# Optimization experiments

Hardware: AMD Instinct MI355X
Metric: run time of the kernel (lower is better)

Reference implementation:

```python
import jax, jax.numpy as jnp
import numpy as np

N_NODES = 50000
N_EDGES = 800000
IN_CH = 128
HID = 16
HEADS = 8
OUT_CH = 40
NEG_SLOPE = 0.2  # PyG GATConv default leaky_relu slope


def segment_softmax(logits, seg, num_segments):
    # logits: [E, H], softmax over edges sharing the same destination node
    m = jax.ops.segment_max(logits, seg, num_segments=num_segments)  # [N, H]
    e = jnp.exp(logits - m[seg])
    s = jax.ops.segment_sum(e, seg, num_segments=num_segments)  # [N, H]
    return e / s[seg]


def gat_conv(x, edge_index, W, att_src, att_dst, bias, heads, ch, concat):
    N = x.shape[0]
    h = (x @ W).reshape(N, heads, ch)                     # [N, H, C]
    a_src = jnp.sum(h * att_src, axis=-1)                 # [N, H]
    a_dst = jnp.sum(h * att_dst, axis=-1)                 # [N, H]
    src, dst = edge_index[0], edge_index[1]
    alpha = jax.nn.leaky_relu(a_src[src] + a_dst[dst], NEG_SLOPE)  # [E, H]
    alpha = segment_softmax(alpha, dst, N)                # [E, H]
    msg = h[src] * alpha[:, :, None]                      # [E, H, C]
    out = jax.ops.segment_sum(msg, dst, num_segments=N)   # [N, H, C]
    out = out.reshape(N, heads * ch) if concat else out.mean(axis=1)
    return out + bias


def setup_inputs() -> dict:
    key = jax.random.key(0)
    ks = jax.random.split(key, 10)
    g = 0.1
    return {
        "x": jax.random.normal(ks[0], (N_NODES, IN_CH), jnp.float32),
        "edge_index": jax.random.randint(ks[1], (2, N_EDGES), 0, N_NODES, jnp.int32),
        "W1": jax.random.normal(ks[2], (IN_CH, HEADS * HID), jnp.float32) * g,
        "att_src1": jax.random.normal(ks[3], (HEADS, HID), jnp.float32) * g,
        "att_dst1": jax.random.normal(ks[4], (HEADS, HID), jnp.float32) * g,
        "b1": jnp.zeros((HEADS * HID,), jnp.float32),
        "W2": jax.random.normal(ks[5], (HEADS * HID, OUT_CH), jnp.float32) * g,
        "att_src2": jax.random.normal(ks[6], (1, OUT_CH), jnp.float32) * g,
        "att_dst2": jax.random.normal(ks[7], (1, OUT_CH), jnp.float32) * g,
        "b2": jnp.zeros((OUT_CH,), jnp.float32),
    }


def reference(x, edge_index, W1, att_src1, att_dst1, b1, W2, att_src2, att_dst2, b2):
    # layer 1: GATConv(in->hid, heads=8, concat) + ELU (dropout is identity in eval)
    h = gat_conv(x, edge_index, W1, att_src1, att_dst1, b1, HEADS, HID, concat=True)
    h = jax.nn.elu(h)
    # layer 2: GATConv(hid*heads->out, heads=1, concat=False)
    out = gat_conv(h, edge_index, W2, att_src2, att_dst2, b2, 1, OUT_CH, concat=False)
    return out
```

## Files before the change

### kernel.cpp

```cpp
#include <hip/hip_runtime.h>
#include <hip/hip_bf16.h>
#include <math.h>

#define N_NODES 50000
#define E_EDGES 800000
#define IN_CH 128
#define HIDX 128
#define OUT_CH 40
#define NEG_SLOPE 0.2f
#define RANK_BLKS 160
#define EDGES_PER_RANK_BLK 5000
#define GEMM_BLKS_X 782
#define PAD_SHIFT 6
#define POISON_I ((int)0xAAAAAAAA)

static __device__ __forceinline__ unsigned int f2bf_pk(float lo, float hi) {
    unsigned int ul = __float_as_uint(lo);
    unsigned int uh = __float_as_uint(hi);
    ul = (ul + 0x7fffu + ((ul >> 16) & 1u)) >> 16;
    uh = (uh + 0x7fffu + ((uh >> 16) & 1u)) >> 16;
    return ul | (uh << 16);
}
static __device__ __forceinline__ float bf2f(unsigned short u) {
    return __uint_as_float(((unsigned int)u) << 16);
}


__global__ __launch_bounds__(256) void gemm1_kernel(
    const float* __restrict__ x, const float* __restrict__ W1,
    const float* __restrict__ as1, const float* __restrict__ ad1,
    unsigned short* __restrict__ H1, float* __restrict__ A1s, float* __restrict__ A1d,
    const int* __restrict__ ei, int* __restrict__ deg, unsigned short* __restrict__ csr_pad)
{
    int tid = threadIdx.x;
    int bid = blockIdx.x;

    if (bid < RANK_BLKS) {
        int start = bid * EDGES_PER_RANK_BLK;
        int endv  = start + EDGES_PER_RANK_BLK;
        if (endv > E_EDGES) endv = E_EDGES;
        for (int base = start; base < endv; base += 1024) {
            int e0 = base + tid;
            int e1 = e0 + 256, e2 = e0 + 512, e3 = e0 + 768;
            bool v0 = e0 < endv, v1 = e1 < endv, v2 = e2 < endv, v3 = e3 < endv;
            int d0 = 0, d1 = 0, d2 = 0, d3 = 0;
            int s0 = 0, s1 = 0, s2 = 0, s3 = 0;
            if (v0) { d0 = ei[E_EDGES + e0]; s0 = ei[e0]; }
            if (v1) { d1 = ei[E_EDGES + e1]; s1 = ei[e1]; }
            if (v2) { d2 = ei[E_EDGES + e2]; s2 = ei[e2]; }
            if (v3) { d3 = ei[E_EDGES + e3]; s3 = ei[e3]; }
            int r0, r1, r2, r3;
            if (v0) r0 = atomicAdd(&deg[d0], 1) - POISON_I;
            if (v1) r1 = atomicAdd(&deg[d1], 1) - POISON_I;
            if (v2) r2 = atomicAdd(&deg[d2], 1) - POISON_I;
            if (v3) r3 = atomicAdd(&deg[d3], 1) - POISON_I;
            if (v0) csr_pad[(d0 << PAD_SHIFT) + r0] = (unsigned short)s0;
            if (v1) csr_pad[(d1 << PAD_SHIFT) + r1] = (unsigned short)s1;
            if (v2) csr_pad[(d2 << PAD_SHIFT) + r2] = (unsigned short)s2;
            if (v3) csr_pad[(d3 << PAD_SHIFT) + r3] = (unsigned short)s3;
        }
        return;
    }

    __shared__ float Ws[32 * 68];
    __shared__ float XT[64 * 40];
    int g = bid - RANK_BLKS;
    int rowbase = (g >> 1) * 64;
    int cb = g & 1;

    const float4* W4 = (const float4*)W1;
    const float4* x4 = (const float4*)x;

    int cg = tid & 15;
    int rg = tid >> 4;
    int c0 = cg * 4;
    int r0 = rg * 4;
    float acc[4][4];
#pragma unroll
    for (int i = 0; i < 4; i++)
#pragma unroll
        for (int j = 0; j < 4; j++) acc[i][j] = 0.f;

#pragma unroll
    for (int kh = 0; kh < 4; kh++) {
        if (kh) __syncthreads();
#pragma unroll
        for (int i = 0; i < 2; i++) {
            int f = i * 256 + tid;
            int k = f >> 4, c4 = f & 15;
            *(float4*)(Ws + k * 68 + c4 * 4) = W4[(kh * 32 + k) * 32 + cb * 16 + c4];
        }
#pragma unroll
        for (int i = 0; i < 2; i++) {
            int f = i * 256 + tid;
            int r = f >> 3, c4 = f & 7;
            int gr = rowbase + r; if (gr >= N_NODES) gr = N_NODES - 1;
            *(float4*)(XT + r * 40 + c4 * 4) = x4[gr * 32 + kh * 8 + c4];
        }
        __syncthreads();

        for (int k = 0; k < 32; k += 4) {
            float4 xv[4];
#pragma unroll
            for (int i = 0; i < 4; i++) xv[i] = *(const float4*)(XT + (r0 + i) * 40 + k);
#pragma unroll
            for (int kk = 0; kk < 4; kk++) {
                float4 wv = *(const float4*)(Ws + (k + kk) * 68 + c0);
#pragma unroll
                for (int i = 0; i < 4; i++) {
                    float xs = (kk == 0) ? xv[i].x : (kk == 1) ? xv[i].y : (kk == 2) ? xv[i].z : xv[i].w;
                    acc[i][0] += xs * wv.x; acc[i][1] += xs * wv.y;
                    acc[i][2] += xs * wv.z; acc[i][3] += xs * wv.w;
                }
            }
        }
    }

    int gc0 = cb * 64 + c0;
    int hh = gc0 >> 4;
    float asp[4] = {0, 0, 0, 0}, adp[4] = {0, 0, 0, 0};
#pragma unroll
    for (int j = 0; j < 4; j++) {
        float va = as1[gc0 + j];
        float vd = ad1[gc0 + j];
#pragma unroll
        for (int i = 0; i < 4; i++) { asp[i] += acc[i][j] * va; adp[i] += acc[i][j] * vd; }
    }
#pragma unroll
    for (int i = 0; i < 4; i++) {
        asp[i] += __shfl_xor(asp[i], 1); asp[i] += __shfl_xor(asp[i], 2);
        adp[i] += __shfl_xor(adp[i], 1); adp[i] += __shfl_xor(adp[i], 2);
    }
#pragma unroll
    for (int i = 0; i < 4; i++) {
        int gr = rowbase + r0 + i;
        if (gr < N_NODES) {
            uint2 v;
            v.x = f2bf_pk(acc[i][0], acc[i][1]);
            v.y = f2bf_pk(acc[i][2], acc[i][3]);
            *(uint2*)(H1 + gr * 128 + gc0) = v;
            if ((cg & 3) == 0) {
                A1s[gr * 8 + hh] = asp[i];
                A1d[gr * 8 + hh] = adp[i];
            }
        }
    }
}


__global__ __launch_bounds__(256) void agg1_kernel(
    const int* __restrict__ deg, const unsigned short* __restrict__ csr_pad,
    const float* __restrict__ A1s, const float* __restrict__ A1d,
    const unsigned short* __restrict__ H1, const float* __restrict__ b1,
    unsigned short* __restrict__ X2)
{
    int gwave = (blockIdx.x * blockDim.x + threadIdx.x) >> 6;
    int lane = threadIdx.x & 63;
    if (gwave >= N_NODES) return;
    int node = gwave;
    int beg = node << PAD_SHIFT;
    int end = beg + (deg[node] - POISON_I);
    int half = lane >> 5;
    int li = lane & 31;
    int head = li >> 2;
    int c0 = li * 4;
    float ad = A1d[node * 8 + head];
    float acc0 = 0.f, acc1 = 0.f, acc2 = 0.f, acc3 = 0.f, sumw = 0.f;
    for (int p = beg; p < end; p += 16) {
        int s[8]; float a[8]; ushort4 u[8]; bool v[8];
#pragma unroll
        for (int t = 0; t < 8; t++) {
            int e = p + 2 * t + half;
            v[t] = e < end;
            s[t] = csr_pad[v[t] ? e : beg];
        }
#pragma unroll
        for (int t = 0; t < 8; t++) a[t] = A1s[s[t] * 8 + head];
#pragma unroll
        for (int t = 0; t < 8; t++) u[t] = *(const ushort4*)(H1 + s[t] * 128 + c0);
#pragma unroll
        for (int t = 0; t < 8; t++) {
            float z = a[t] + ad; z = z >= 0.f ? z : NEG_SLOPE * z;
            float w = v[t] ? __expf(z) : 0.f;
            acc0 += w * bf2f(u[t].x);
            acc1 += w * bf2f(u[t].y);
            acc2 += w * bf2f(u[t].z);
            acc3 += w * bf2f(u[t].w);
            sumw += w;
        }
    }
    acc0 += __shfl_xor(acc0, 32);
    acc1 += __shfl_xor(acc1, 32);
    acc2 += __shfl_xor(acc2, 32);
    acc3 += __shfl_xor(acc3, 32);
    sumw += __shfl_xor(sumw, 32);
    if (half == 0) {
        float inv = (end > beg) ? 1.0f / sumw : 0.0f;
        float4 bv = *(const float4*)(b1 + c0);
        float o0 = acc0 * inv + bv.x;
        float o1 = acc1 * inv + bv.y;
        float o2 = acc2 * inv + bv.z;
        float o3 = acc3 * inv + bv.w;
        o0 = o0 > 0.f ? o0 : expm1f(o0);
        o1 = o1 > 0.f ? o1 : expm1f(o1);
        o2 = o2 > 0.f ? o2 : expm1f(o2);
        o3 = o3 > 0.f ? o3 : expm1f(o3);
        uint2 ov;
        ov.x = f2bf_pk(o0, o1);
        ov.y = f2bf_pk(o2, o3);
        *(uint2*)(X2 + node * 128 + c0) = ov;
    }
}


__global__ __launch_bounds__(256) void gemm2_kernel(
    const unsigned short* __restrict__ X2, const float* __restrict__ W2,
    const float* __restrict__ as2, const float* __restrict__ ad2,
    unsigned short* __restrict__ H2, float* __restrict__ A2s, float* __restrict__ A2d)
{
    __shared__ float Ws[128 * 40];
    __shared__ float XS[64 * 132];
    int tid = threadIdx.x;
    int rowbase = blockIdx.x * 64;

#pragma unroll
    for (int i = 0; i < 20; i++) Ws[i * 256 + tid] = W2[i * 256 + tid];

    const uint2* x2v = (const uint2*)X2;
#pragma unroll
    for (int i = 0; i < 8; i++) {
        int f = i * 256 + tid;
        int r = f >> 5, c4 = f & 31;
        int gr = rowbase + r; if (gr >= N_NODES) gr = N_NODES - 1;
        uint2 pk = x2v[gr * 32 + c4];
        float* dst = XS + r * 132 + c4 * 4;
        dst[0] = bf2f((unsigned short)(pk.x & 0xffff));
        dst[1] = bf2f((unsigned short)(pk.x >> 16));
        dst[2] = bf2f((unsigned short)(pk.y & 0xffff));
        dst[3] = bf2f((unsigned short)(pk.y >> 16));
    }
    __syncthreads();

    int q = tid & 3, r = tid >> 2;
    float acc[10];
#pragma unroll
    for (int j = 0; j < 10; j++) acc[j] = 0.f;
    for (int k = 0; k < 128; k += 4) {
        float4 xv = *(const float4*)(XS + r * 132 + k);
#pragma unroll
        for (int kk = 0; kk < 4; kk++) {
            float xs = (kk == 0) ? xv.x : (kk == 1) ? xv.y : (kk == 2) ? xv.z : xv.w;
#pragma unroll
            for (int j = 0; j < 10; j++) acc[j] += xs * Ws[(k + kk) * 40 + q * 10 + j];
        }
    }
    float asum = 0.f, dsum = 0.f;
#pragma unroll
    for (int j = 0; j < 10; j++) {
        asum += acc[j] * as2[q * 10 + j];
        dsum += acc[j] * ad2[q * 10 + j];
    }
    asum += __shfl_xor(asum, 1); asum += __shfl_xor(asum, 2);
    dsum += __shfl_xor(dsum, 1); dsum += __shfl_xor(dsum, 2);
    int gr = rowbase + r;
    if (gr < N_NODES) {
#pragma unroll
        for (int t = 0; t < 5; t++)
            *(unsigned int*)(H2 + gr * 40 + q * 10 + t * 2) = f2bf_pk(acc[t * 2], acc[t * 2 + 1]);
        if (q == 0) { A2s[gr] = asum; A2d[gr] = dsum; }
    }
}


__global__ __launch_bounds__(256) void agg2_kernel(
    const int* __restrict__ deg, const unsigned short* __restrict__ csr_pad,
    const float* __restrict__ A2s, const float* __restrict__ A2d,
    const unsigned short* __restrict__ H2, const float* __restrict__ b2,
    float* __restrict__ out)
{
    int gwave = (blockIdx.x * blockDim.x + threadIdx.x) >> 6;
    int lane = threadIdx.x & 63;
    if (gwave >= N_NODES) return;
    int node = gwave;
    int beg = node << PAD_SHIFT;
    int end = beg + (deg[node] - POISON_I);
    int half = lane >> 5;
    int li = lane & 31;
    bool act = li < 20;
    int c0 = li * 2;
    int cc = act ? c0 : 0;
    float ad = A2d[node];
    float acc0 = 0.f, acc1 = 0.f, sumw = 0.f;
    for (int p = beg; p < end; p += 16) {
        int s[8]; float a[8]; ushort2 u[8]; bool v[8];
#pragma unroll
        for (int t = 0; t < 8; t++) {
            int e = p + 2 * t + half;
            v[t] = e < end;
            s[t] = csr_pad[v[t] ? e : beg];
        }
#pragma unroll
        for (int t = 0; t < 8; t++) a[t] = A2s[s[t]];
#pragma unroll
        for (int t = 0; t < 8; t++) u[t] = *(const ushort2*)(H2 + s[t] * OUT_CH + cc);
#pragma unroll
        for (int t = 0; t < 8; t++) {
            float z = a[t] + ad; z = z >= 0.f ? z : NEG_SLOPE * z;
            float w = v[t] ? __expf(z) : 0.f;
            acc0 += w * bf2f(u[t].x);
            acc1 += w * bf2f(u[t].y);
            sumw += w;
        }
    }
    acc0 += __shfl_xor(acc0, 32);
    acc1 += __shfl_xor(acc1, 32);
    sumw += __shfl_xor(sumw, 32);
    if (half == 0 && act) {
        float inv = (end > beg) ? 1.0f / sumw : 0.0f;
        float o0 = acc0 * inv + b2[c0];
        float o1 = acc1 * inv + b2[c0 + 1];
        float2 ov = {o0, o1};
        *(float2*)(out + node * OUT_CH + c0) = ov;
    }
}


extern "C" void kernel_launch(void* const* d_in, const int* in_sizes, int n_in,
                              void* d_out, int out_size, void* d_ws, size_t ws_size,
                              hipStream_t stream) {
    const float* x   = (const float*)d_in[0];
    const int*   ei  = (const int*)d_in[1];
    const float* W1  = (const float*)d_in[2];
    const float* as1 = (const float*)d_in[3];
    const float* ad1 = (const float*)d_in[4];
    const float* b1  = (const float*)d_in[5];
    const float* W2  = (const float*)d_in[6];
    const float* as2 = (const float*)d_in[7];
    const float* ad2 = (const float*)d_in[8];
    const float* b2  = (const float*)d_in[9];
    float* out = (float*)d_out;

    char* ws = (char*)d_ws;
    size_t off = 0;
    auto alloc = [&](size_t bytes) {
        void* p = ws + off;
        off += (bytes + 255) & ~size_t(255);
        return p;
    };
    unsigned short* H1 = (unsigned short*)alloc((size_t)N_NODES * 128 * 2);
    unsigned short* X2 = (unsigned short*)alloc((size_t)N_NODES * 128 * 2);
    unsigned short* H2 = (unsigned short*)alloc((size_t)N_NODES * OUT_CH * 2);
    float* A1s    = (float*)alloc((size_t)N_NODES * 8 * 4);
    float* A1d    = (float*)alloc((size_t)N_NODES * 8 * 4);
    float* A2s    = (float*)alloc((size_t)N_NODES * 4);
    float* A2d    = (float*)alloc((size_t)N_NODES * 4);
    int* deg      = (int*)alloc((size_t)N_NODES * 4);
    unsigned short* csr_pad = (unsigned short*)alloc((size_t)N_NODES * 64 * 2);


    gemm1_kernel<<<RANK_BLKS + GEMM_BLKS_X * 2, 256, 0, stream>>>(
        x, W1, as1, ad1, H1, A1s, A1d, ei, deg, csr_pad);

    agg1_kernel<<<(N_NODES + 3) / 4, 256, 0, stream>>>(deg, csr_pad, A1s, A1d, H1, b1, X2);

    gemm2_kernel<<<(N_NODES + 63) / 64, 256, 0, stream>>>(X2, W2, as2, ad2, H2, A2s, A2d);
    agg2_kernel<<<(N_NODES + 3) / 4, 256, 0, stream>>>(deg, csr_pad, A2s, A2d, H2, b2, out);
}
```

Measured before the change: 217.5 us.

## Fuse layer-1 aggregation with layer-2 GEMM through shared memory

Merges the layer-1 attention aggregation and the layer-2 projection into one kernel: each block aggregates 32 nodes (8 per wave) into bf16 rows in LDS, then multiplies them by a transposed W2 tile held in LDS. This removes the X2 global round trip and one kernel launch. In exchange each block does more serial work per wave, reloads and transposes W2 in every block, and uses more shared memory, which may lower occupancy for the latency-bound gather phase.

```diff
diff --git a/kernel.cpp b/kernel.cpp
--- a/kernel.cpp
+++ b/kernel.cpp
@@ -11,6 +11,7 @@
 #define RANK_BLKS 160
 #define EDGES_PER_RANK_BLK 5000
 #define GEMM_BLKS_X 782
+#define FUSE_BLKS 1563
 #define PAD_SHIFT 6
 #define POISON_I ((int)0xAAAAAAAA)
 
@@ -20,6 +21,10 @@
     ul = (ul + 0x7fffu + ((ul >> 16) & 1u)) >> 16;
     uh = (uh + 0x7fffu + ((uh >> 16) & 1u)) >> 16;
     return ul | (uh << 16);
+}
+static __device__ __forceinline__ unsigned short f2bf1(float v) {
+    unsigned int u = __float_as_uint(v);
+    return (unsigned short)((u + 0x7fffu + ((u >> 16) & 1u)) >> 16);
 }
 static __device__ __forceinline__ float bf2f(unsigned short u) {
     return __uint_as_float(((unsigned int)u) << 16);
@@ -71,9 +76,9 @@
     const float4* W4 = (const float4*)W1;
     const float4* x4 = (const float4*)x;
 
-    int cg = tid & 15;
+    int cg_ = tid & 15;
     int rg = tid >> 4;
-    int c0 = cg * 4;
+    int c0 = cg_ * 4;
     int r0 = rg * 4;
     float acc[4][4];
 #pragma unroll
@@ -139,7 +144,7 @@
             v.x = f2bf_pk(acc[i][0], acc[i][1]);
             v.y = f2bf_pk(acc[i][2], acc[i][3]);
             *(uint2*)(H1 + gr * 128 + gc0) = v;
-            if ((cg & 3) == 0) {
+            if ((cg_ & 3) == 0) {
                 A1s[gr * 8 + hh] = asp[i];
                 A1d[gr * 8 + hh] = adp[i];
             }
@@ -148,126 +153,132 @@
 }
 
 
-__global__ __launch_bounds__(256) void agg1_kernel(
+__global__ __launch_bounds__(256) void fused_ag_kernel(
     const int* __restrict__ deg, const unsigned short* __restrict__ csr_pad,
     const float* __restrict__ A1s, const float* __restrict__ A1d,
     const unsigned short* __restrict__ H1, const float* __restrict__ b1,
-    unsigned short* __restrict__ X2)
+    const float* __restrict__ W2, const float* __restrict__ as2,
+    const float* __restrict__ ad2,
+    unsigned short* __restrict__ H2, float* __restrict__ A2s, float* __restrict__ A2d)
 {
-    int gwave = (blockIdx.x * blockDim.x + threadIdx.x) >> 6;
-    int lane = threadIdx.x & 63;
-    if (gwave >= N_NODES) return;
-    int node = gwave;
-    int beg = node << PAD_SHIFT;
-    int end = beg + (deg[node] - POISON_I);
+    __shared__ float WsT[40 * 132];
+    __shared__ unsigned int x2s[32 * 68];
+    int tid = threadIdx.x;
+    int bid = blockIdx.x;
+    int wid = tid >> 6;
+    int lane = tid & 63;
     int half = lane >> 5;
     int li = lane & 31;
-    int head = li >> 2;
-    int c0 = li * 4;
-    float ad = A1d[node * 8 + head];
-    float acc0 = 0.f, acc1 = 0.f, acc2 = 0.f, acc3 = 0.f, sumw = 0.f;
-    for (int p = beg; p < end; p += 16) {
-        int s[8]; float a[8]; ushort4 u[8]; bool v[8];
-#pragma unroll
-        for (int t = 0; t < 8; t++) {
-            int e = p + 2 * t + half;
-            v[t] = e < end;
-            s[t] = csr_pad[v[t] ? e : beg];
-        }
-#pragma unroll
-        for (int t = 0; t < 8; t++) a[t] = A1s[s[t] * 8 + head];
-#pragma unroll
-        for (int t = 0; t < 8; t++) u[t] = *(const ushort4*)(H1 + s[t] * 128 + c0);
-#pragma unroll
-        for (int t = 0; t < 8; t++) {
-            float z = a[t] + ad; z = z >= 0.f ? z : NEG_SLOPE * z;
-            float w = v[t] ? __expf(z) : 0.f;
-            acc0 += w * bf2f(u[t].x);
-            acc1 += w * bf2f(u[t].y);
-            acc2 += w * bf2f(u[t].z);
-            acc3 += w * bf2f(u[t].w);
-            sumw += w;
-        }
-    }
-    acc0 += __shfl_xor(acc0, 32);
-    acc1 += __shfl_xor(acc1, 32);
-    acc2 += __shfl_xor(acc2, 32);
-    acc3 += __shfl_xor(acc3, 32);
-    sumw += __shfl_xor(sumw, 32);
-    if (half == 0) {
-        float inv = (end > beg) ? 1.0f / sumw : 0.0f;
-        float4 bv = *(const float4*)(b1 + c0);
-        float o0 = acc0 * inv + bv.x;
-        float o1 = acc1 * inv + bv.y;
-        float o2 = acc2 * inv + bv.z;
-        float o3 = acc3 * inv + bv.w;
-        o0 = o0 > 0.f ? o0 : expm1f(o0);
-        o1 = o1 > 0.f ? o1 : expm1f(o1);
-        o2 = o2 > 0.f ? o2 : expm1f(o2);
-        o3 = o3 > 0.f ? o3 : expm1f(o3);
-        uint2 ov;
-        ov.x = f2bf_pk(o0, o1);
-        ov.y = f2bf_pk(o2, o3);
-        *(uint2*)(X2 + node * 128 + c0) = ov;
-    }
-}
-
-
-__global__ __launch_bounds__(256) void gemm2_kernel(
-    const unsigned short* __restrict__ X2, const float* __restrict__ W2,
-    const float* __restrict__ as2, const float* __restrict__ ad2,
-    unsigned short* __restrict__ H2, float* __restrict__ A2s, float* __restrict__ A2d)
-{
-    __shared__ float Ws[128 * 40];
-    __shared__ float XS[64 * 132];
-    int tid = threadIdx.x;
-    int rowbase = blockIdx.x * 64;
-
-#pragma unroll
-    for (int i = 0; i < 20; i++) Ws[i * 256 + tid] = W2[i * 256 + tid];
-
-    const uint2* x2v = (const uint2*)X2;
-#pragma unroll
-    for (int i = 0; i < 8; i++) {
+    int rowbase = bid * 32;
+
+    {
+        int head = li >> 2;
+        int c0 = li * 4;
+#pragma unroll
+        for (int i = 0; i < 8; i++) {
+            int nl = wid * 8 + i;
+            int node = rowbase + nl;
+            if (node < N_NODES) {
+                int beg = node << PAD_SHIFT;
+                int end = beg + (deg[node] - POISON_I);
+                float ad = A1d[node * 8 + head];
+                float acc0 = 0.f, acc1 = 0.f, acc2 = 0.f, acc3 = 0.f, sumw = 0.f;
+                for (int p = beg; p < end; p += 16) {
+                    int s[8]; float a[8]; ushort4 u[8]; bool v[8];
+#pragma unroll
+                    for (int t = 0; t < 8; t++) {
+                        int e = p + 2 * t + half;
+                        v[t] = e < end;
+                        s[t] = csr_pad[v[t] ? e : beg];
+                    }
+#pragma unroll
+                    for (int t = 0; t < 8; t++) a[t] = A1s[s[t] * 8 + head];
+#pragma unroll
+                    for (int t = 0; t < 8; t++) u[t] = *(const ushort4*)(H1 + s[t] * 128 + c0);
+#pragma unroll
+                    for (int t = 0; t < 8; t++) {
+                        float z = a[t] + ad; z = z >= 0.f ? z : NEG_SLOPE * z;
+                        float w = v[t] ? __expf(z) : 0.f;
+                        acc0 += w * bf2f(u[t].x);
+                        acc1 += w * bf2f(u[t].y);
+                        acc2 += w * bf2f(u[t].z);
+                        acc3 += w * bf2f(u[t].w);
+                        sumw += w;
+                    }
+                }
+                acc0 += __shfl_xor(acc0, 32);
+                acc1 += __shfl_xor(acc1, 32);
+                acc2 += __shfl_xor(acc2, 32);
+                acc3 += __shfl_xor(acc3, 32);
+                sumw += __shfl_xor(sumw, 32);
+                if (half == 0) {
+                    float inv = (end > beg) ? 1.0f / sumw : 0.0f;
+                    float4 bv = *(const float4*)(b1 + c0);
+                    float o0 = acc0 * inv + bv.x;
+                    float o1 = acc1 * inv + bv.y;
+                    float o2 = acc2 * inv + bv.z;
+                    float o3 = acc3 * inv + bv.w;
+                    o0 = o0 > 0.f ? o0 : expm1f(o0);
+                    o1 = o1 > 0.f ? o1 : expm1f(o1);
+                    o2 = o2 > 0.f ? o2 : expm1f(o2);
+                    o3 = o3 > 0.f ? o3 : expm1f(o3);
+                    uint2 ov;
+                    ov.x = f2bf_pk(o0, o1);
+                    ov.y = f2bf_pk(o2, o3);
+                    *(uint2*)(&x2s[nl * 68 + li * 2]) = ov;
+                }
+            }
+        }
+    }
+
+#pragma unroll
+    for (int i = 0; i < 20; i++) {
         int f = i * 256 + tid;
-        int r = f >> 5, c4 = f & 31;
-        int gr = rowbase + r; if (gr >= N_NODES) gr = N_NODES - 1;
-        uint2 pk = x2v[gr * 32 + c4];
-        float* dst = XS + r * 132 + c4 * 4;
-        dst[0] = bf2f((unsigned short)(pk.x & 0xffff));
-        dst[1] = bf2f((unsigned short)(pk.x >> 16));
-        dst[2] = bf2f((unsigned short)(pk.y & 0xffff));
-        dst[3] = bf2f((unsigned short)(pk.y >> 16));
+        int c = f >> 7, k = f & 127;
+        WsT[c * 132 + k] = W2[k * 40 + c];
     }
     __syncthreads();
 
-    int q = tid & 3, r = tid >> 2;
-    float acc[10];
-#pragma unroll
-    for (int j = 0; j < 10; j++) acc[j] = 0.f;
-    for (int k = 0; k < 128; k += 4) {
-        float4 xv = *(const float4*)(XS + r * 132 + k);
-#pragma unroll
-        for (int kk = 0; kk < 4; kk++) {
-            float xs = (kk == 0) ? xv.x : (kk == 1) ? xv.y : (kk == 2) ? xv.z : xv.w;
-#pragma unroll
-            for (int j = 0; j < 10; j++) acc[j] += xs * Ws[(k + kk) * 40 + q * 10 + j];
-        }
-    }
-    float asum = 0.f, dsum = 0.f;
-#pragma unroll
-    for (int j = 0; j < 10; j++) {
-        asum += acc[j] * as2[q * 10 + j];
-        dsum += acc[j] * ad2[q * 10 + j];
-    }
-    asum += __shfl_xor(asum, 1); asum += __shfl_xor(asum, 2);
-    dsum += __shfl_xor(dsum, 1); dsum += __shfl_xor(dsum, 2);
-    int gr = rowbase + r;
-    if (gr < N_NODES) {
-#pragma unroll
-        for (int t = 0; t < 5; t++)
-            *(unsigned int*)(H2 + gr * 40 + q * 10 + t * 2) = f2bf_pk(acc[t * 2], acc[t * 2 + 1]);
-        if (q == 0) { A2s[gr] = asum; A2d[gr] = dsum; }
+    {
+        int q = tid & 7;
+        int rr = tid >> 3;
+        int c0q = q * 5;
+        int gr = rowbase + rr;
+
+        float acc[5];
+#pragma unroll
+        for (int j = 0; j < 5; j++) acc[j] = 0.f;
+
+        for (int kc = 0; kc < 16; kc++) {
+            uint4 pa = *(const uint4*)(&x2s[rr * 68 + kc * 4]);
+            float xa[8];
+            xa[0] = __uint_as_float(pa.x << 16); xa[1] = __uint_as_float(pa.x & 0xffff0000u);
+            xa[2] = __uint_as_float(pa.y << 16); xa[3] = __uint_as_float(pa.y & 0xffff0000u);
+            xa[4] = __uint_as_float(pa.z << 16); xa[5] = __uint_as_float(pa.z & 0xffff0000u);
+            xa[6] = __uint_as_float(pa.w << 16); xa[7] = __uint_as_float(pa.w & 0xffff0000u);
+#pragma unroll
+            for (int j = 0; j < 5; j++) {
+                float4 w0 = *(const float4*)(WsT + (c0q + j) * 132 + kc * 8);
+                float4 w1 = *(const float4*)(WsT + (c0q + j) * 132 + kc * 8 + 4);
+                acc[j] += xa[0] * w0.x + xa[1] * w0.y + xa[2] * w0.z + xa[3] * w0.w
+                        + xa[4] * w1.x + xa[5] * w1.y + xa[6] * w1.z + xa[7] * w1.w;
+            }
+        }
+
+        float as0 = 0.f, ds0 = 0.f;
+#pragma unroll
+        for (int j = 0; j < 5; j++) {
+            float va = as2[c0q + j], vd = ad2[c0q + j];
+            as0 += acc[j] * va; ds0 += acc[j] * vd;
+        }
+        as0 += __shfl_xor(as0, 1); as0 += __shfl_xor(as0, 2); as0 += __shfl_xor(as0, 4);
+        ds0 += __shfl_xor(ds0, 1); ds0 += __shfl_xor(ds0, 2); ds0 += __shfl_xor(ds0, 4);
+
+        if (gr < N_NODES) {
+#pragma unroll
+            for (int j = 0; j < 5; j++) H2[gr * OUT_CH + c0q + j] = f2bf1(acc[j]);
+            if (q == 0) { A2s[gr] = as0; A2d[gr] = ds0; }
+        }
     }
 }
 
@@ -348,7 +359,6 @@
         return p;
     };
     unsigned short* H1 = (unsigned short*)alloc((size_t)N_NODES * 128 * 2);
-    unsigned short* X2 = (unsigned short*)alloc((size_t)N_NODES * 128 * 2);
     unsigned short* H2 = (unsigned short*)alloc((size_t)N_NODES * OUT_CH * 2);
     float* A1s    = (float*)alloc((size_t)N_NODES * 8 * 4);
     float* A1d    = (float*)alloc((size_t)N_NODES * 8 * 4);
@@ -361,8 +371,8 @@
     gemm1_kernel<<<RANK_BLKS + GEMM_BLKS_X * 2, 256, 0, stream>>>(
         x, W1, as1, ad1, H1, A1s, A1d, ei, deg, csr_pad);
 
-    agg1_kernel<<<(N_NODES + 3) / 4, 256, 0, stream>>>(deg, csr_pad, A1s, A1d, H1, b1, X2);
-
-    gemm2_kernel<<<(N_NODES + 63) / 64, 256, 0, stream>>>(X2, W2, as2, ad2, H2, A2s, A2d);
+    fused_ag_kernel<<<FUSE_BLKS, 256, 0, stream>>>(
+        deg, csr_pad, A1s, A1d, H1, b1, W2, as2, ad2, H2, A2s, A2d);
+
     agg2_kernel<<<(N_NODES + 3) / 4, 256, 0, stream>>>(deg, csr_pad, A2s, A2d, H2, b2, out);
 }
```

Measured after the change: 227.9 us. 4.8% more time.
